# Optimization experiments

Measured on AMD Instinct MI355X. Metric: run time of the kernel, lower is better.

## Reference

```python
import jax, jax.numpy as jnp
import numpy as np

T, B, IN, H, OUT = 512, 128, 64, 1024, 64


def _gru_layer(x, w_ih, w_hh, b_ih, b_hh):
    # x: (T, B, in_dim); w_ih: (3H, in_dim); w_hh: (3H, H); gate order: r, z, n (torch)
    gi = jnp.einsum('tbi,gi->tbg', x, w_ih) + b_ih  # (T, B, 3H) input-side gates, precomputed
    h0 = jnp.zeros((x.shape[1], w_hh.shape[1]), x.dtype)

    def step(h, gi_t):
        gh = h @ w_hh.T + b_hh                      # (B, 3H)
        ir, iz, inn = jnp.split(gi_t, 3, axis=-1)
        hr, hz, hn = jnp.split(gh, 3, axis=-1)
        r = jax.nn.sigmoid(ir + hr)
        z = jax.nn.sigmoid(iz + hz)
        n = jnp.tanh(inn + r * hn)
        h_new = (1.0 - z) * n + z * h
        return h_new, h_new

    _, out = jax.lax.scan(step, h0, gi)             # out: (T, B, H)
    return out


def setup_inputs() -> dict:
    key = jax.random.key(0)
    ks = jax.random.split(key, 11)
    s_in = 1.0 / np.sqrt(H)
    inp = {
        'x': jax.random.normal(ks[0], (T, B, IN), dtype=jnp.float32),
        'w_ih0': jax.random.uniform(ks[1], (3 * H, IN), jnp.float32, -s_in, s_in),
        'w_hh0': jax.random.uniform(ks[2], (3 * H, H), jnp.float32, -s_in, s_in),
        'b_ih0': jax.random.uniform(ks[3], (3 * H,), jnp.float32, -s_in, s_in),
        'b_hh0': jax.random.uniform(ks[4], (3 * H,), jnp.float32, -s_in, s_in),
        'w_ih1': jax.random.uniform(ks[5], (3 * H, H), jnp.float32, -s_in, s_in),
        'w_hh1': jax.random.uniform(ks[6], (3 * H, H), jnp.float32, -s_in, s_in),
        'b_ih1': jax.random.uniform(ks[7], (3 * H,), jnp.float32, -s_in, s_in),
        'b_hh1': jax.random.uniform(ks[8], (3 * H,), jnp.float32, -s_in, s_in),
        'w_lin': jax.random.uniform(ks[9], (OUT, H), jnp.float32, -s_in, s_in),
        'b_lin': jax.random.uniform(ks[10], (OUT,), jnp.float32, -s_in, s_in),
    }
    return inp


def reference(x, w_ih0, w_hh0, b_ih0, b_hh0, w_ih1, w_hh1, b_ih1, b_hh1, w_lin, b_lin):
    h1 = _gru_layer(x, w_ih0, w_hh0, b_ih0, b_hh0)   # (T, B, H)
    h2 = _gru_layer(h1, w_ih1, w_hh1, b_ih1, b_hh1)  # (T, B, H)
    out = jnp.einsum('tbh,oh->tbo', h2, w_lin) + b_lin  # time-distributed linear
    return out
```

## Files before the change

kernel.cpp:

```cpp
#include <hip/hip_runtime.h>

#define Tn  512
#define Bn  128
#define INn 64
#define Hn  1024

typedef __attribute__((ext_vector_type(8))) _Float16 f16x8;
typedef __attribute__((ext_vector_type(4))) float f32x4;
typedef unsigned short u16;

#define AGENT __HIP_MEMORY_SCOPE_AGENT

__device__ __forceinline__ u16 f2h(float f) {
  union { _Float16 h; u16 u; } v;
  v.h = (_Float16)f;
  return v.u;
}
__device__ __forceinline__ float sigmoidf_(float x) {
  return 1.0f / (1.0f + __expf(-x));
}
__device__ __forceinline__ float tanhf_(float x) {
  float e = __expf(-2.0f * fabsf(x));
  float t = (1.0f - e) / (1.0f + e);
  return copysignf(t, x);
}
__device__ __forceinline__ f32x4 mfma16(f16x8 a, f16x8 b, f32x4 c) {
  return __builtin_amdgcn_mfma_f32_16x16x32_f16(a, b, c, 0, 0, 0);
}
__device__ __forceinline__ size_t hidx(int row, int col) {
  return ((size_t)((row >> 4) * 32 + (col >> 5))) * 512 +
         ((((col >> 3) & 3) * 16 + (row & 15)) * 8) + (col & 7);
}
__device__ __forceinline__ void acq_fence() {
  __builtin_amdgcn_fence(__ATOMIC_ACQUIRE, "agent");
}
__device__ __forceinline__ void coh_store(u16* p, u16 a, u16 b) {
  __hip_atomic_store((unsigned*)p, (unsigned)a | ((unsigned)b << 16),
                     __ATOMIC_RELAXED, AGENT);
}
__device__ __forceinline__ void ldb4(f16x8 dst[4], const u16* __restrict__ h,
                                     size_t ab, int kc0) {
#pragma unroll
  for (int k = 0; k < 4; ++k)
    dst[k] = *(const f16x8*)(h + ab + (size_t)(kc0 + k) * 512);
}
__device__ __forceinline__ void fma12(f32x4 acc[3], const f16x8 b[4],
                                      const f16x8 W[3][8], int kc0) {
#pragma unroll
  for (int k = 0; k < 4; ++k) {
#pragma unroll
    for (int g = 0; g < 3; ++g)
      acc[g] = mfma16(b[k], W[g][kc0 + k], acc[g]);
  }
}

__global__ void pack_w(const float* __restrict__ s, u16* __restrict__ d, int R, int K) {
  int tid = blockIdx.x * blockDim.x + threadIdx.x;
  int total = (R * K) >> 3;
  if (tid >= total) return;
  int l = tid & 63;
  int ckc = tid >> 6;
  int nkc = K >> 5;
  int ct = ckc / nkc;
  int kc = ckc - ct * nkc;
  int row = ct * 16 + (l & 15);
  int k0 = kc * 32 + (l >> 4) * 8;
  const float* sp = s + (size_t)row * K + k0;
  float4 a = *(const float4*)sp;
  float4 b = *(const float4*)(sp + 4);
  f16x8 o;
  u16* op = (u16*)&o;
  op[0] = f2h(a.x); op[1] = f2h(a.y); op[2] = f2h(a.z); op[3] = f2h(a.w);
  op[4] = f2h(b.x); op[5] = f2h(b.y); op[6] = f2h(b.z); op[7] = f2h(b.w);
  *(f16x8*)(d + (size_t)tid * 8) = o;
}

__global__ void zero16(uint4* __restrict__ p, int n4) {
  int i = blockIdx.x * blockDim.x + threadIdx.x;
  if (i < n4) p[i] = make_uint4(0u, 0u, 0u, 0u);
}

#define PS 131072

__global__ __launch_bounds__(512, 1) void gru_main(
    const float* __restrict__ x,
    const float* __restrict__ b_ih0, const float* __restrict__ b_hh0,
    const float* __restrict__ b_ih1, const float* __restrict__ b_hh1,
    const float* __restrict__ b_lin,
    const u16* __restrict__ wih0p, const u16* __restrict__ whh0p,
    const u16* __restrict__ wih1p, const u16* __restrict__ whh1p,
    const u16* __restrict__ wlinp,
    u16* __restrict__ hA, u16* __restrict__ hB,
    float* __restrict__ out, int* __restrict__ flags) {
  extern __shared__ float lds[];

  const int blk  = blockIdx.x;
  const int tid  = threadIdx.x;
  const int w    = tid >> 6;
  const int lane = tid & 63;
  const int ln   = lane & 15;
  const int lq   = lane >> 4;
  const int layer = blk >> 7;
  const int lb   = blk & 127;
  const f32x4 vz = {0.f, 0.f, 0.f, 0.f};

  if (layer == 0) {
    const int bg  = lb >> 5;
    const int hsl = lb & 31;
    const int q   = w & 1;
    const int kg  = w >> 1;
    const int c16 = hsl * 2 + q;
    const bool kgl = (kg < 2);
    const int xm  = kg;
    f16x8 W[3][8];
#pragma unroll
    for (int g = 0; g < 3; ++g)
#pragma unroll
      for (int kc = 0; kc < 8; ++kc)
        W[g][kc] = *(const f16x8*)(whh0p + (((size_t)(g * 64 + c16) * 32 + kg * 8 + kc) * 64 + lane) * 8);
    f16x8 Wx[3][2];
    if (kgl) {
#pragma unroll
      for (int g = 0; g < 3; ++g)
#pragma unroll
        for (int kc = 0; kc < 2; ++kc)
          Wx[g][kc] = *(const f16x8*)(wih0p + (((size_t)(g * 64 + c16) * 2 + kc) * 64 + lane) * 8);
    }
    const bool is_lin = (hsl < 8);
    const int lcg = hsl & 3;
    const int lrt = hsl >> 2;
    float Blin = 0.f;
    f16x8 Wl[4];
    if (is_lin) {
      Blin = b_lin[lcg * 16 + (tid & 15)];
#pragma unroll
      for (int kc = 0; kc < 4; ++kc)
        Wl[kc] = *(const f16x8*)(wlinp + (((size_t)lcg * 32 + w * 4 + kc) * 64 + lane) * 8);
    }
    const int rm  = tid >> 8;
    const int rr  = (tid >> 4) & 15;
    const int rc2 = (tid & 15) * 2;
    const int ggr = bg * 32 + rm * 16 + rr;
    float Br[2], Bz[2], Bni[2], Bnh[2];
#pragma unroll
    for (int e = 0; e < 2; ++e) {
      const int gc = hsl * 32 + rc2 + e;
      Br[e]  = b_ih0[gc] + b_hh0[gc];
      Bz[e]  = b_ih0[Hn + gc] + b_hh0[Hn + gc];
      Bni[e] = b_ih0[2 * Hn + gc];
      Bnh[e] = b_hh0[2 * Hn + gc];
    }
    const int* pPeer = flags + ((bg << 5) + (lane & 31)) * 32;
    const int* pBp   = flags + 4096 + (((bg >> 1) << 6) + lane) * 32;
    const size_t abL = ((size_t)(bg * 2 + lrt) * 32 + w * 4) * 512 + lane * 8;
    float h0prev[2] = {0.f, 0.f};

    for (int t = 0; t <= Tn + 3; ++t) {
      f16x8 lbuf[4];
      if (t < Tn) {
        if (w == 0) {
          for (;;) {
            bool ok = true;
            if (t > 0 && __hip_atomic_load(pPeer, __ATOMIC_RELAXED, AGENT) < t) ok = false;
            if (t >= 4 && __hip_atomic_load(pBp, __ATOMIC_RELAXED, AGENT) < t - 3) ok = false;
            if (!__all(ok)) { __builtin_amdgcn_s_sleep(1); continue; }
            break;
          }
          acq_fence();
        }
        __syncthreads();
        const int rs = (t + 3) & 3;
        const int ws_ = t & 3;
        const u16* Ahb = hA + (size_t)rs * PS;
        float4 xv0, xv1, xv2, xv3;
        if (kgl) {
          const float* xr = x + ((size_t)t * Bn + bg * 32 + xm * 16 + ln) * INn + lq * 8;
          xv0 = *(const float4*)xr;        xv1 = *(const float4*)(xr + 4);
          xv2 = *(const float4*)(xr + 32); xv3 = *(const float4*)(xr + 36);
        }
        f32x4 acc0[3] = {vz, vz, vz}, acc1[3] = {vz, vz, vz};
        f16x8 b0[4], b1[4], b2[4], b3[4];
        const size_t ab0 = ((size_t)(bg * 2 + 0) * 32 + kg * 8) * 512 + lane * 8;
        const size_t ab1 = ((size_t)(bg * 2 + 1) * 32 + kg * 8) * 512 + lane * 8;
        ldb4(b0, Ahb, ab0, 0);
        ldb4(b1, Ahb, ab0, 4);
        ldb4(b2, Ahb, ab1, 0);
        ldb4(b3, Ahb, ab1, 4);
        if (is_lin && t >= 4)
          ldb4(lbuf, hB + (size_t)((t - 4) & 3) * PS, abL, 0);
        fma12(acc0, b0, W, 0);
        fma12(acc0, b1, W, 4);
        fma12(acc1, b2, W, 0);
        fma12(acc1, b3, W, 4);
        {
          float* Hp0 = lds + (size_t)(0 * 4 + kg) * 1632;
          float* Hp1 = lds + (size_t)(1 * 4 + kg) * 1632;
#pragma unroll
          for (int g = 0; g < 3; ++g)
#pragma unroll
            for (int i = 0; i < 4; ++i) {
              Hp0[g * 544 + (lq * 4 + i) * 34 + q * 16 + ln] = acc0[g][i];
              Hp1[g * 544 + (lq * 4 + i) * 34 + q * 16 + ln] = acc1[g][i];
            }
        }
        if (kgl) {
          f16x8 a0, a1;
          u16* a0p = (u16*)&a0;
          u16* a1p = (u16*)&a1;
          a0p[0] = f2h(xv0.x); a0p[1] = f2h(xv0.y); a0p[2] = f2h(xv0.z); a0p[3] = f2h(xv0.w);
          a0p[4] = f2h(xv1.x); a0p[5] = f2h(xv1.y); a0p[6] = f2h(xv1.z); a0p[7] = f2h(xv1.w);
          a1p[0] = f2h(xv2.x); a1p[1] = f2h(xv2.y); a1p[2] = f2h(xv2.z); a1p[3] = f2h(xv2.w);
          a1p[4] = f2h(xv3.x); a1p[5] = f2h(xv3.y); a1p[6] = f2h(xv3.z); a1p[7] = f2h(xv3.w);
          f32x4 ax[3] = {vz, vz, vz};
#pragma unroll
          for (int g = 0; g < 3; ++g) {
            ax[g] = mfma16(a0, Wx[g][0], ax[g]);
            ax[g] = mfma16(a1, Wx[g][1], ax[g]);
          }
          float* Ip = lds + 13056 + (size_t)xm * 1632;
#pragma unroll
          for (int g = 0; g < 3; ++g)
#pragma unroll
            for (int i = 0; i < 4; ++i)
              Ip[g * 544 + (lq * 4 + i) * 34 + q * 16 + ln] = ax[g][i];
        }
        __syncthreads();
        {
          u16* whp = hA + (size_t)ws_ * PS;
          const size_t idx0 = hidx(ggr, hsl * 32 + rc2);
          u16 hh[2];
#pragma unroll
          for (int e = 0; e < 2; ++e) {
            const int c = rc2 + e;
            const float* Ip = lds + 13056 + (size_t)rm * 1632 + rr * 34 + c;
            float I0 = Ip[0], I1 = Ip[544], I2 = Ip[1088];
            float H0 = 0.f, H1 = 0.f, H2 = 0.f;
#pragma unroll
            for (int kgi = 0; kgi < 4; ++kgi) {
              const float* Hp = lds + (size_t)(rm * 4 + kgi) * 1632 + rr * 34 + c;
              H0 += Hp[0]; H1 += Hp[544]; H2 += Hp[1088];
            }
            float r  = sigmoidf_(I0 + H0 + Br[e]);
            float zz = sigmoidf_(I1 + H1 + Bz[e]);
            float nn = tanhf_(I2 + Bni[e] + r * (H2 + Bnh[e]));
            float hv = (1.0f - zz) * nn + zz * h0prev[e];
            h0prev[e] = hv;
            hh[e] = f2h(hv);
          }
          coh_store(whp + idx0, hh[0], hh[1]);
        }
        __syncthreads();
        if (tid == 0)
          __hip_atomic_store(flags + ((bg << 5) + hsl) * 32, t + 1, __ATOMIC_RELAXED, AGENT);
      } else if (is_lin) {
        if (w == 0) {
          while (!__all(__hip_atomic_load(pBp, __ATOMIC_RELAXED, AGENT) >= t - 3))
            __builtin_amdgcn_s_sleep(1);
          acq_fence();
        }
        __syncthreads();
        ldb4(lbuf, hB + (size_t)((t - 4) & 3) * PS, abL, 0);
      }
      if (is_lin && t >= 4) {
        const int s2 = t - 4;
        f32x4 la = vz;
#pragma unroll
        for (int k = 0; k < 4; ++k)
          la = mfma16(lbuf[k], Wl[k], la);
        __syncthreads();
        if (tid == 0)
          __hip_atomic_store(flags + 8192 + ((bg << 3) + hsl) * 32, s2 + 1, __ATOMIC_RELAXED, AGENT);
#pragma unroll
        for (int i = 0; i < 4; ++i)
          lds[(w * 16 + lq * 4 + i) * 20 + ln] = la[i];
        __syncthreads();
        if (tid < 256) {
          const int lr = (tid >> 4) & 15, lc = tid & 15;
          float s = Blin;
#pragma unroll
          for (int w8 = 0; w8 < 8; ++w8)
            s += lds[(w8 * 16 + lr) * 20 + lc];
          out[((size_t)s2 * Bn + bg * 32 + lrt * 16 + lr) * 64 + lcg * 16 + lc] = s;
        }
      }
    }
  } else {
    const int cs  = lb >> 1;
    const int rh  = lb & 1;
    const int side = w >> 2;
    const int ks  = w & 3;
    const u16* wsrc = side ? whh1p : wih1p;
    f16x8 W[3][8];
#pragma unroll
    for (int g = 0; g < 3; ++g)
#pragma unroll
      for (int kc = 0; kc < 8; ++kc)
        W[g][kc] = *(const f16x8*)(wsrc + (((size_t)(g * 64 + cs) * 32 + ks * 8 + kc) * 64 + lane) * 8);
    const int mq  = tid >> 7;
    const int er  = (tid >> 3) & 15;
    const int ec0 = (tid & 7) * 2;
    float Br2[2], Bz2[2], Bni2[2], Bnh2[2];
#pragma unroll
    for (int e = 0; e < 2; ++e) {
      const int g2 = cs * 16 + ec0 + e;
      Br2[e]  = b_ih1[g2] + b_hh1[g2];
      Bz2[e]  = b_ih1[Hn + g2] + b_hh1[Hn + g2];
      Bni2[e] = b_ih1[2 * Hn + g2];
      Bnh2[e] = b_hh1[2 * Hn + g2];
    }
    const size_t idxE = hidx(rh * 64 + mq * 16 + er, cs * 16 + ec0);
    float h1prev[2] = {0.f, 0.f};
    const int* pA = flags + ((rh << 6) + lane) * 32;
    const int* pB = flags + 4096 + ((rh << 6) + lane) * 32;
    const int* pC = flags + 8192 + ((rh << 4) + (lane & 15)) * 32;

    for (int s = 0; s < Tn; ++s) {
      if (w == 0) {
        for (;;) {
          bool ok = __hip_atomic_load(pA, __ATOMIC_RELAXED, AGENT) >= s + 1;
          if (s >= 4 && (lane & 15) == lane &&
              __hip_atomic_load(pC, __ATOMIC_RELAXED, AGENT) < s - 3) ok = false;
          if (__all(ok)) break;
          __builtin_amdgcn_s_sleep(1);
        }
        acq_fence();
      }
      __syncthreads();
      const int ss = s & 3;
      const int rs = (s + 3) & 3;
      const u16* A1h = hA + (size_t)ss * PS;
      const u16* A2h = hB + (size_t)rs * PS;
      u16* whp = hB + (size_t)ss * PS;
      const u16* Ahb = side ? A2h : A1h;
      if (side && s > 0) {
        while (!__all(__hip_atomic_load(pB, __ATOMIC_RELAXED, AGENT) >= s))
          __builtin_amdgcn_s_sleep(1);
      }
      f32x4 acc0[3] = {vz, vz, vz}, acc1[3] = {vz, vz, vz};
      f32x4 acc2[3] = {vz, vz, vz}, acc3[3] = {vz, vz, vz};
      f16x8 b0[4], b1[4], b2[4], b3[4];
      const int mA = rh * 4;
      const size_t abT0 = ((size_t)(mA + 0) * 32 + ks * 8) * 512 + lane * 8;
      const size_t abT1 = ((size_t)(mA + 1) * 32 + ks * 8) * 512 + lane * 8;
      const size_t abT2 = ((size_t)(mA + 2) * 32 + ks * 8) * 512 + lane * 8;
      const size_t abT3 = ((size_t)(mA + 3) * 32 + ks * 8) * 512 + lane * 8;
      ldb4(b0, Ahb, abT0, 0);
      ldb4(b1, Ahb, abT0, 4);
      ldb4(b2, Ahb, abT1, 0);
      ldb4(b3, Ahb, abT1, 4);
      fma12(acc0, b0, W, 0);
      ldb4(b0, Ahb, abT2, 0);
      fma12(acc0, b1, W, 4);
      ldb4(b1, Ahb, abT2, 4);
      fma12(acc1, b2, W, 0);
      ldb4(b2, Ahb, abT3, 0);
      fma12(acc1, b3, W, 4);
      ldb4(b3, Ahb, abT3, 4);
      fma12(acc2, b0, W, 0);
      fma12(acc2, b1, W, 4);
      fma12(acc3, b2, W, 0);
      fma12(acc3, b3, W, 4);
#pragma unroll
      for (int g = 0; g < 3; ++g)
#pragma unroll
        for (int i = 0; i < 4; ++i) {
          const int ro = (lq * 4 + i) * 20 + ln;
          lds[((0 * 8 + w) * 3 + g) * 320 + ro] = acc0[g][i];
          lds[((1 * 8 + w) * 3 + g) * 320 + ro] = acc1[g][i];
          lds[((2 * 8 + w) * 3 + g) * 320 + ro] = acc2[g][i];
          lds[((3 * 8 + w) * 3 + g) * 320 + ro] = acc3[g][i];
        }
      __syncthreads();
      {
        u16 hh[2];
#pragma unroll
        for (int e = 0; e < 2; ++e) {
          const int rc = ec0 + e;
          float I0 = 0.f, I1 = 0.f, I2 = 0.f, H0 = 0.f, H1 = 0.f, H2 = 0.f;
#pragma unroll
          for (int wi = 0; wi < 4; ++wi) {
            const float* P = lds + ((mq * 8 + wi) * 3) * 320 + er * 20 + rc;
            I0 += P[0]; I1 += P[320]; I2 += P[640];
          }
#pragma unroll
          for (int wi = 4; wi < 8; ++wi) {
            const float* P = lds + ((mq * 8 + wi) * 3) * 320 + er * 20 + rc;
            H0 += P[0]; H1 += P[320]; H2 += P[640];
          }
          float r  = sigmoidf_(I0 + H0 + Br2[e]);
          float zz = sigmoidf_(I1 + H1 + Bz2[e]);
          float nn = tanhf_(I2 + Bni2[e] + r * (H2 + Bnh2[e]));
          float hv = (1.0f - zz) * nn + zz * h1prev[e];
          h1prev[e] = hv;
          hh[e] = f2h(hv);
        }
        coh_store(whp + idxE, hh[0], hh[1]);
      }
      __syncthreads();
      if (tid == 0)
        __hip_atomic_store(flags + 4096 + ((rh << 6) + cs) * 32, s + 1, __ATOMIC_RELAXED, AGENT);
    }
  }
}

extern "C" void kernel_launch(void* const* d_in, const int* in_sizes, int n_in,
                              void* d_out, int out_size, void* d_ws, size_t ws_size,
                              hipStream_t stream) {
  (void)in_sizes; (void)n_in; (void)out_size; (void)ws_size;
  const float* x     = (const float*)d_in[0];
  const float* wih0f = (const float*)d_in[1];
  const float* whh0f = (const float*)d_in[2];
  const float* bih0  = (const float*)d_in[3];
  const float* bhh0  = (const float*)d_in[4];
  const float* wih1f = (const float*)d_in[5];
  const float* whh1f = (const float*)d_in[6];
  const float* bih1  = (const float*)d_in[7];
  const float* bhh1  = (const float*)d_in[8];
  const float* wlinf = (const float*)d_in[9];
  const float* blin  = (const float*)d_in[10];
  float* out = (float*)d_out;

  char* w = (char*)d_ws;
  u16* whh0p = (u16*)w; w += (size_t)3072 * 1024 * 2;
  u16* wih1p = (u16*)w; w += (size_t)3072 * 1024 * 2;
  u16* whh1p = (u16*)w; w += (size_t)3072 * 1024 * 2;
  u16* wih0p = (u16*)w; w += (size_t)3072 * 64 * 2;
  u16* wlinp = (u16*)w; w += (size_t)64 * 1024 * 2;
  u16* hA    = (u16*)w; w += (size_t)4 * PS * 2;
  u16* hB    = (u16*)w; w += (size_t)4 * PS * 2;
  int* flags = (int*)w; w += 36864;

  static int attr_done = 0;
  if (!attr_done) {
    (void)hipFuncSetAttribute((const void*)gru_main,
                              hipFuncAttributeMaxDynamicSharedMemorySize, 131072);
    attr_done = 1;
  }

  const int thr = 256;
  pack_w<<<(3072 * 1024 / 8 + thr - 1) / thr, thr, 0, stream>>>(whh0f, whh0p, 3072, 1024);
  pack_w<<<(3072 * 1024 / 8 + thr - 1) / thr, thr, 0, stream>>>(wih1f, wih1p, 3072, 1024);
  pack_w<<<(3072 * 1024 / 8 + thr - 1) / thr, thr, 0, stream>>>(whh1f, whh1p, 3072, 1024);
  pack_w<<<(3072 * 64 / 8 + thr - 1) / thr, thr, 0, stream>>>(wih0f, wih0p, 3072, 64);
  pack_w<<<(64 * 1024 / 8 + thr - 1) / thr, thr, 0, stream>>>(wlinf, wlinp, 64, 1024);
  const int n4 = (int)(((size_t)8 * PS * 2 + 36864) / 16);
  zero16<<<(n4 + thr - 1) / thr, thr, 0, stream>>>((uint4*)hA, n4);

  void* args[] = {(void*)&x,     (void*)&bih0,  (void*)&bhh0,  (void*)&bih1,  (void*)&bhh1,
                  (void*)&blin,  (void*)&wih0p, (void*)&whh0p, (void*)&wih1p, (void*)&whh1p,
                  (void*)&wlinp, (void*)&hA,    (void*)&hB,    (void*)&out,   (void*)&flags};
  hipLaunchCooperativeKernel((const void*)gru_main, dim3(256), dim3(512), args, 122880, stream);
}
```

Baseline: 4.041 ms.

## Replace per-block flag arrays with shared atomic counters for cross-block sync

Each producer block used to write its own step flag, and consumers polled up to 64 flags per wave with __all. Now producers atomically increment one shared counter per group, and consumers poll a single counter against a scaled threshold (32*t, 64*(t-3), and so on). This cuts the number of polled cache lines and the wave-wide reductions in the spin loops. In exchange, every producer in a group does an atomic add on the same line, which can contend. The flag buffer also has to be zeroed at the start of every launch.

```diff
diff --git a/kernel.cpp b/kernel.cpp
--- a/kernel.cpp
+++ b/kernel.cpp
@@ -37,6 +37,12 @@
 __device__ __forceinline__ void coh_store(u16* p, u16 a, u16 b) {
   __hip_atomic_store((unsigned*)p, (unsigned)a | ((unsigned)b << 16),
                      __ATOMIC_RELAXED, AGENT);
+}
+__device__ __forceinline__ int ctr_ld(const int* p) {
+  return __hip_atomic_load(p, __ATOMIC_RELAXED, AGENT);
+}
+__device__ __forceinline__ void ctr_add(int* p) {
+  __hip_atomic_fetch_add(p, 1, __ATOMIC_RELAXED, AGENT);
 }
 __device__ __forceinline__ void ldb4(f16x8 dst[4], const u16* __restrict__ h,
                                      size_t ab, int kc0) {
@@ -150,8 +156,9 @@
       Bni[e] = b_ih0[2 * Hn + gc];
       Bnh[e] = b_hh0[2 * Hn + gc];
     }
-    const int* pPeer = flags + ((bg << 5) + (lane & 31)) * 32;
-    const int* pBp   = flags + 4096 + (((bg >> 1) << 6) + lane) * 32;
+    int* ctrA  = flags + bg * 32;
+    const int* ctrBh = flags + 1024 + (bg >> 1) * 32;
+    int* ctrC  = flags + 2048 + (bg >> 1) * 32;
     const size_t abL = ((size_t)(bg * 2 + lrt) * 32 + w * 4) * 512 + lane * 8;
     float h0prev[2] = {0.f, 0.f};
 
@@ -159,12 +166,14 @@
       f16x8 lbuf[4];
       if (t < Tn) {
         if (w == 0) {
+          const int thrA = 32 * t;
+          const int thrB = 64 * (t - 3);
           for (;;) {
             bool ok = true;
-            if (t > 0 && __hip_atomic_load(pPeer, __ATOMIC_RELAXED, AGENT) < t) ok = false;
-            if (t >= 4 && __hip_atomic_load(pBp, __ATOMIC_RELAXED, AGENT) < t - 3) ok = false;
-            if (!__all(ok)) { __builtin_amdgcn_s_sleep(1); continue; }
-            break;
+            if (t > 0 && ctr_ld(ctrA) < thrA) ok = false;
+            if (t >= 4 && ctr_ld(ctrBh) < thrB) ok = false;
+            if (ok) break;
+            __builtin_amdgcn_s_sleep(1);
           }
           acq_fence();
         }
@@ -250,11 +259,10 @@
           coh_store(whp + idx0, hh[0], hh[1]);
         }
         __syncthreads();
-        if (tid == 0)
-          __hip_atomic_store(flags + ((bg << 5) + hsl) * 32, t + 1, __ATOMIC_RELAXED, AGENT);
+        if (tid == 0) ctr_add(ctrA);
       } else if (is_lin) {
         if (w == 0) {
-          while (!__all(__hip_atomic_load(pBp, __ATOMIC_RELAXED, AGENT) >= t - 3))
+          while (ctr_ld(ctrBh) < 64 * (t - 3))
             __builtin_amdgcn_s_sleep(1);
           acq_fence();
         }
@@ -268,8 +276,7 @@
         for (int k = 0; k < 4; ++k)
           la = mfma16(lbuf[k], Wl[k], la);
         __syncthreads();
-        if (tid == 0)
-          __hip_atomic_store(flags + 8192 + ((bg << 3) + hsl) * 32, s2 + 1, __ATOMIC_RELAXED, AGENT);
+        if (tid == 0) ctr_add(ctrC);
 #pragma unroll
         for (int i = 0; i < 4; ++i)
           lds[(w * 16 + lq * 4 + i) * 20 + ln] = la[i];
@@ -310,17 +317,19 @@
     }
     const size_t idxE = hidx(rh * 64 + mq * 16 + er, cs * 16 + ec0);
     float h1prev[2] = {0.f, 0.f};
-    const int* pA = flags + ((rh << 6) + lane) * 32;
-    const int* pB = flags + 4096 + ((rh << 6) + lane) * 32;
-    const int* pC = flags + 8192 + ((rh << 4) + (lane & 15)) * 32;
+    const int* ctrA0 = flags + (2 * rh + 0) * 32;
+    const int* ctrA1 = flags + (2 * rh + 1) * 32;
+    int*       ctrB  = flags + 1024 + rh * 32;
+    const int* ctrC  = flags + 2048 + rh * 32;
 
     for (int s = 0; s < Tn; ++s) {
       if (w == 0) {
+        const int thrA = 32 * (s + 1);
+        const int thrC = 16 * (s - 3);
         for (;;) {
-          bool ok = __hip_atomic_load(pA, __ATOMIC_RELAXED, AGENT) >= s + 1;
-          if (s >= 4 && (lane & 15) == lane &&
-              __hip_atomic_load(pC, __ATOMIC_RELAXED, AGENT) < s - 3) ok = false;
-          if (__all(ok)) break;
+          bool ok = (ctr_ld(ctrA0) >= thrA) && (ctr_ld(ctrA1) >= thrA);
+          if (s >= 4 && ctr_ld(ctrC) < thrC) ok = false;
+          if (ok) break;
           __builtin_amdgcn_s_sleep(1);
         }
         acq_fence();
@@ -333,7 +342,7 @@
       u16* whp = hB + (size_t)ss * PS;
       const u16* Ahb = side ? A2h : A1h;
       if (side && s > 0) {
-        while (!__all(__hip_atomic_load(pB, __ATOMIC_RELAXED, AGENT) >= s))
+        while (ctr_ld(ctrB) < 64 * s)
           __builtin_amdgcn_s_sleep(1);
       }
       f32x4 acc0[3] = {vz, vz, vz}, acc1[3] = {vz, vz, vz};
@@ -397,8 +406,7 @@
         coh_store(whp + idxE, hh[0], hh[1]);
       }
       __syncthreads();
-      if (tid == 0)
-        __hip_atomic_store(flags + 4096 + ((rh << 6) + cs) * 32, s + 1, __ATOMIC_RELAXED, AGENT);
+      if (tid == 0) ctr_add(ctrB);
     }
   }
 }
```

Result: slower. 4.635 ms (+14.7%).
